# Optimization experiments

Measured on AMD Instinct MI355X. Metric: run time of the kernel, lower is better.

## Reference

```python
import jax, jax.numpy as jnp
import numpy as np

BETA = 0.9
THRESH = 1.0
ALPHA = 2.0  # snntorch ATan surrogate default

@jax.custom_vjp
def atan_spike(x):
    return (x > 0).astype(x.dtype)

def _atan_fwd(x):
    return atan_spike(x), x

def _atan_bwd(x, g):
    # d/dx of snntorch ATan surrogate: (alpha/2) / (1 + (pi/2*alpha*x)^2)
    return (g * (ALPHA / 2) / (1 + (jnp.pi / 2 * ALPHA * x) ** 2),)

atan_spike.defvjp(_atan_fwd, _atan_bwd)

def setup_inputs() -> dict:
    key = jax.random.key(0)
    k1, k2, k3, k4, k5 = jax.random.split(key, 5)
    B, T, F, H, O = 256, 1024, 64, 512, 64
    x = jax.random.normal(k1, (B, T, F), dtype=jnp.float32)
    s_in = 1.0 / np.sqrt(F)
    s_out = 1.0 / np.sqrt(H)
    W_in = jax.random.uniform(k2, (H, F), jnp.float32, -s_in, s_in)
    b_in = jax.random.uniform(k3, (H,), jnp.float32, -s_in, s_in)
    W_out = jax.random.uniform(k4, (O, H), jnp.float32, -s_out, s_out)
    b_out = jax.random.uniform(k5, (O,), jnp.float32, -s_out, s_out)
    return {"x": x, "W_in": W_in, "b_in": b_in, "W_out": W_out, "b_out": b_out}

def reference(x, W_in, b_in, W_out, b_out):
    B, T, F = x.shape
    H = W_in.shape[0]
    O = W_out.shape[0]
    dt = x.dtype
    # precompute input currents for all steps: [T, B, H]
    cur1_all = jnp.einsum('btf,hf->tbh', x, W_in) + b_in

    def step(carry, cur1):
        mem1, mem_out = carry
        # snntorch Leaky(subtract): reset from previous mem (detached),
        # then mem = beta*mem + input - reset*threshold, spike from new mem.
        reset1 = jax.lax.stop_gradient((mem1 > THRESH).astype(dt))
        mem1 = BETA * mem1 + cur1 - reset1 * THRESH
        spk1 = atan_spike(mem1 - THRESH)
        cur_out = spk1 @ W_out.T + b_out
        reset_o = jax.lax.stop_gradient((mem_out > THRESH).astype(dt))
        mem_out = BETA * mem_out + cur_out - reset_o * THRESH
        spk_out = atan_spike(mem_out - THRESH)
        return (mem1, mem_out), (mem_out, spk_out)

    init = (jnp.zeros((B, H), dt), jnp.zeros((B, O), dt))
    _, (mem_rec, spk_rec) = jax.lax.scan(step, init, cur1_all)
    # [T, B, O] -> [B, T, O]
    return mem_rec.transpose(1, 0, 2), spk_rec.transpose(1, 0, 2)
```

## Files before the change

### kernel.cpp

```cpp
#include <hip/hip_runtime.h>


typedef __attribute__((ext_vector_type(16))) float f32x16;

namespace {
constexpr int kB = 256;
constexpr int kT = 1024;
constexpr int kF = 64;
constexpr int kH = 512;
constexpr int kO = 64;
constexpr float kBeta = 0.9f;
constexpr float kThresh = 1.0f;
constexpr int kThreads = 512;
}

#define XV(i) ((i) < 16 ? sx0[(i)] : (i) < 32 ? sx1[(i)-16] \
             : (i) < 48 ? sx2[(i)-32] : sx3[(i)-48])
#define BITF(k) ((((k) < 32 ? (mlo >> (k)) : (mhi >> ((k)-32))) & 1u) \
                 ? 1.0f : 0.0f)

__global__ __launch_bounds__(kThreads, 2)
void snn_fused2(const float* __restrict__ x,
                const float* __restrict__ W_in,
                const float* __restrict__ b_in,
                const float* __restrict__ W_out,
                const float* __restrict__ b_out,
                float* __restrict__ out) {
  const int b = blockIdx.x;
  const int j = threadIdx.x;
  const int o = j & 63;
  const int s = j >> 6;

  __shared__ float red[2][8][64];

  float win[kF];
#pragma unroll
  for (int q = 0; q < 16; ++q) {
    const float4 v = *reinterpret_cast<const float4*>(W_in + j * kF + q * 4);
    win[q * 4 + 0] = v.x; win[q * 4 + 1] = v.y;
    win[q * 4 + 2] = v.z; win[q * 4 + 3] = v.w;
  }
  float wout[64];
#pragma unroll
  for (int q = 0; q < 16; ++q) {
    const float4 v =
        *reinterpret_cast<const float4*>(W_out + o * kH + s * 64 + q * 4);
    wout[q * 4 + 0] = v.x; wout[q * 4 + 1] = v.y;
    wout[q * 4 + 2] = v.z; wout[q * 4 + 3] = v.w;
  }
  const float bin_j = b_in[j];
  const float bout_o = b_out[o];

  float mem1 = 0.0f, rst1 = 0.0f;
  float memo = 0.0f, rsto = 0.0f;
  unsigned long long mask = 0ull;

  const float* xrow = x + (size_t)b * kT * kF;
  float* out_mem = out + (size_t)b * kT * kO + o;
  float* out_spk = out_mem + (size_t)kB * kT * kO;

  f32x16 sx0, sx1, sx2, sx3;

#define ISSUE_X(tt)                                                        \
  do {                                                                     \
    const float* xp = xrow + (size_t)(tt) * kF;                            \
    asm volatile("s_load_dwordx16 %0, %4, 0x0\n\t"                         \
                 "s_load_dwordx16 %1, %4, 0x40\n\t"                        \
                 "s_load_dwordx16 %2, %4, 0x80\n\t"                        \
                 "s_load_dwordx16 %3, %4, 0xc0"                            \
                 : "=&s"(sx0), "=&s"(sx1), "=&s"(sx2), "=&s"(sx3)          \
                 : "s"(xp));                                               \
  } while (0)

#define BARRIER() asm volatile("s_waitcnt lgkmcnt(0)\n\ts_barrier" ::: "memory")

#define PIN_X()                                                            \
  asm volatile("s_waitcnt lgkmcnt(0)"                                      \
               : "+s"(sx0), "+s"(sx1), "+s"(sx2), "+s"(sx3)::"memory")

#define LAYER1()                                                           \
  do {                                                                     \
    float c0 = bin_j, c1 = 0.0f, c2 = 0.0f, c3 = 0.0f;                     \
    _Pragma("unroll") for (int q = 0; q < 16; ++q) {                       \
      c0 = fmaf(XV(4 * q + 0), win[4 * q + 0], c0);                        \
      c1 = fmaf(XV(4 * q + 1), win[4 * q + 1], c1);                        \
      c2 = fmaf(XV(4 * q + 2), win[4 * q + 2], c2);                        \
      c3 = fmaf(XV(4 * q + 3), win[4 * q + 3], c3);                        \
    }                                                                      \
    const float cur1 = (c0 + c1) + (c2 + c3);                              \
    mem1 = kBeta * mem1 + cur1 - rst1;                                     \
    const bool p = mem1 > kThresh;                                         \
    mask = __ballot(p);                                                    \
    rst1 = p ? 1.0f : 0.0f;                                                \
  } while (0)

#define LAYER2(buf)                                                        \
  do {                                                                     \
    const unsigned mlo = (unsigned)mask;                                   \
    const unsigned mhi = (unsigned)(mask >> 32);                           \
    float a0 = 0.0f, a1 = 0.0f, a2 = 0.0f, a3 = 0.0f;                      \
    _Pragma("unroll") for (int q = 0; q < 16; ++q) {                       \
      a0 = fmaf(BITF(4 * q + 0), wout[4 * q + 0], a0);                     \
      a1 = fmaf(BITF(4 * q + 1), wout[4 * q + 1], a1);                     \
      a2 = fmaf(BITF(4 * q + 2), wout[4 * q + 2], a2);                     \
      a3 = fmaf(BITF(4 * q + 3), wout[4 * q + 3], a3);                     \
    }                                                                      \
    red[(buf)][s][o] = (a0 + a1) + (a2 + a3);                              \
  } while (0)

  ISSUE_X(0);
  BARRIER();
  PIN_X();
  LAYER1();

  for (int t = 1; t < kT; ++t) {
    ISSUE_X(t);
    LAYER2((t - 1) & 1);
    BARRIER();
    PIN_X();

    {
      const int buf = (t - 1) & 1;
      float co = bout_o;
#pragma unroll
      for (int s2 = 0; s2 < 8; ++s2) co += red[buf][s2][o];
      memo = kBeta * memo + co - rsto;
      const float so = (memo > kThresh) ? 1.0f : 0.0f;
      rsto = so;
      if (j < kO) {
        out_mem[(t - 1) * kO] = memo;
        out_spk[(t - 1) * kO] = so;
      }
    }

    LAYER1();
  }

  LAYER2((kT - 1) & 1);
  BARRIER();
  {
    const int buf = (kT - 1) & 1;
    float co = bout_o;
#pragma unroll
    for (int s2 = 0; s2 < 8; ++s2) co += red[buf][s2][o];
    memo = kBeta * memo + co - rsto;
    const float so = (memo > kThresh) ? 1.0f : 0.0f;
    if (j < kO) {
      out_mem[(kT - 1) * kO] = memo;
      out_spk[(kT - 1) * kO] = so;
    }
  }

#undef ISSUE_X
#undef BARRIER
#undef PIN_X
#undef LAYER1
#undef LAYER2
}

extern "C" void kernel_launch(void* const* d_in, const int* in_sizes, int n_in,
                              void* d_out, int out_size, void* d_ws,
                              size_t ws_size, hipStream_t stream) {
  const float* x = (const float*)d_in[0];
  const float* W_in = (const float*)d_in[1];
  const float* b_in = (const float*)d_in[2];
  const float* W_out = (const float*)d_in[3];
  const float* b_out = (const float*)d_in[4];
  float* out = (float*)d_out;

  hipLaunchKernelGGL(snn_fused2, dim3(kB), dim3(kThreads), 0, stream,
                     x, W_in, b_in, W_out, b_out, out);
}
```

Baseline: 1.169 ms.

## Prefetch x via vector loads one step ahead and pre-warm cache with a read kernel

Replaces the per-step scalar s_load_dwordx16 fetch of x with 16 float4 vector loads per thread, issued one timestep ahead so the loads overlap the layer-2 work and the barrier. A separate warm-up kernel first streams all of x through the cache so the recurrent kernel's loads hit in L2/MALL. Weights are pinned to registers with empty asm statements, and the output reduction is limited to the first wave instead of being computed by every thread. Every thread now holds 64 extra VGPRs for the x copy, which can raise register pressure, and the warm-up kernel adds a full extra read pass over x.

```diff
diff --git a/kernel.cpp b/kernel.cpp
--- a/kernel.cpp
+++ b/kernel.cpp
@@ -1,7 +1,5 @@
 #include <hip/hip_runtime.h>
 
-
-typedef __attribute__((ext_vector_type(16))) float f32x16;
 
 namespace {
 constexpr int kB = 256;
@@ -14,13 +12,22 @@
 constexpr int kThreads = 512;
 }
 
-#define XV(i) ((i) < 16 ? sx0[(i)] : (i) < 32 ? sx1[(i)-16] \
-             : (i) < 48 ? sx2[(i)-32] : sx3[(i)-48])
+__global__ __launch_bounds__(256)
+void warm_x_kernel(const float4* __restrict__ p, int n4) {
+  float acc = 0.0f;
+  for (int i = blockIdx.x * blockDim.x + threadIdx.x; i < n4;
+       i += gridDim.x * blockDim.x) {
+    const float4 v = p[i];
+    acc += v.x + v.y + v.z + v.w;
+  }
+  asm volatile("" ::"v"(acc));
+}
+
 #define BITF(k) ((((k) < 32 ? (mlo >> (k)) : (mhi >> ((k)-32))) & 1u) \
                  ? 1.0f : 0.0f)
 
 __global__ __launch_bounds__(kThreads, 2)
-void snn_fused2(const float* __restrict__ x,
+void snn_fused4(const float* __restrict__ x,
                 const float* __restrict__ W_in,
                 const float* __restrict__ b_in,
                 const float* __restrict__ W_out,
@@ -34,59 +41,72 @@
   __shared__ float red[2][8][64];
 
   float win[kF];
+  {
+    const float4* wiv = reinterpret_cast<const float4*>(W_in) + j * 16;
 #pragma unroll
-  for (int q = 0; q < 16; ++q) {
-    const float4 v = *reinterpret_cast<const float4*>(W_in + j * kF + q * 4);
-    win[q * 4 + 0] = v.x; win[q * 4 + 1] = v.y;
-    win[q * 4 + 2] = v.z; win[q * 4 + 3] = v.w;
+    for (int q = 0; q < 16; ++q) {
+      const float4 v = wiv[q];
+      win[4 * q + 0] = v.x; win[4 * q + 1] = v.y;
+      win[4 * q + 2] = v.z; win[4 * q + 3] = v.w;
+    }
   }
   float wout[64];
+  {
+    const float4* wov =
+        reinterpret_cast<const float4*>(W_out) + o * 128 + s * 16;
 #pragma unroll
-  for (int q = 0; q < 16; ++q) {
-    const float4 v =
-        *reinterpret_cast<const float4*>(W_out + o * kH + s * 64 + q * 4);
-    wout[q * 4 + 0] = v.x; wout[q * 4 + 1] = v.y;
-    wout[q * 4 + 2] = v.z; wout[q * 4 + 3] = v.w;
+    for (int q = 0; q < 16; ++q) {
+      const float4 v = wov[q];
+      wout[4 * q + 0] = v.x; wout[4 * q + 1] = v.y;
+      wout[4 * q + 2] = v.z; wout[4 * q + 3] = v.w;
+    }
   }
-  const float bin_j = b_in[j];
-  const float bout_o = b_out[o];
+  float bin_j = b_in[j];
+  float bout_o = b_out[o];
+
+#define PIN8(p)                                                            \
+  asm volatile("" : "+v"((p)[0]), "+v"((p)[1]), "+v"((p)[2]),              \
+                    "+v"((p)[3]), "+v"((p)[4]), "+v"((p)[5]),              \
+                    "+v"((p)[6]), "+v"((p)[7]))
+  PIN8(win + 0);  PIN8(win + 8);  PIN8(win + 16); PIN8(win + 24);
+  PIN8(win + 32); PIN8(win + 40); PIN8(win + 48); PIN8(win + 56);
+  PIN8(wout + 0);  PIN8(wout + 8);  PIN8(wout + 16); PIN8(wout + 24);
+  PIN8(wout + 32); PIN8(wout + 40); PIN8(wout + 48); PIN8(wout + 56);
+#undef PIN8
+  asm volatile("" : "+v"(bin_j), "+v"(bout_o));
 
   float mem1 = 0.0f, rst1 = 0.0f;
   float memo = 0.0f, rsto = 0.0f;
   unsigned long long mask = 0ull;
 
-  const float* xrow = x + (size_t)b * kT * kF;
+  const float4* xv = reinterpret_cast<const float4*>(x + (size_t)b * kT * kF);
   float* out_mem = out + (size_t)b * kT * kO + o;
   float* out_spk = out_mem + (size_t)kB * kT * kO;
 
-  f32x16 sx0, sx1, sx2, sx3;
+  float4 x0, x1, x2, x3, x4, x5, x6, x7, x8, x9, x10, x11, x12, x13, x14, x15;
 
-#define ISSUE_X(tt)                                                        \
+#define LOADX(tt)                                                          \
   do {                                                                     \
-    const float* xp = xrow + (size_t)(tt) * kF;                            \
-    asm volatile("s_load_dwordx16 %0, %4, 0x0\n\t"                         \
-                 "s_load_dwordx16 %1, %4, 0x40\n\t"                        \
-                 "s_load_dwordx16 %2, %4, 0x80\n\t"                        \
-                 "s_load_dwordx16 %3, %4, 0xc0"                            \
-                 : "=&s"(sx0), "=&s"(sx1), "=&s"(sx2), "=&s"(sx3)          \
-                 : "s"(xp));                                               \
+    const float4* xp = xv + (size_t)(tt) * 16;                             \
+    x0 = xp[0]; x1 = xp[1]; x2 = xp[2]; x3 = xp[3];                        \
+    x4 = xp[4]; x5 = xp[5]; x6 = xp[6]; x7 = xp[7];                        \
+    x8 = xp[8]; x9 = xp[9]; x10 = xp[10]; x11 = xp[11];                    \
+    x12 = xp[12]; x13 = xp[13]; x14 = xp[14]; x15 = xp[15];                \
   } while (0)
 
 #define BARRIER() asm volatile("s_waitcnt lgkmcnt(0)\n\ts_barrier" ::: "memory")
 
-#define PIN_X()                                                            \
-  asm volatile("s_waitcnt lgkmcnt(0)"                                      \
-               : "+s"(sx0), "+s"(sx1), "+s"(sx2), "+s"(sx3)::"memory")
+#define L1Q(q)                                                             \
+  c0 = fmaf(x##q.x, win[4 * q + 0], c0);                                   \
+  c1 = fmaf(x##q.y, win[4 * q + 1], c1);                                   \
+  c2 = fmaf(x##q.z, win[4 * q + 2], c2);                                   \
+  c3 = fmaf(x##q.w, win[4 * q + 3], c3);
 
 #define LAYER1()                                                           \
   do {                                                                     \
     float c0 = bin_j, c1 = 0.0f, c2 = 0.0f, c3 = 0.0f;                     \
-    _Pragma("unroll") for (int q = 0; q < 16; ++q) {                       \
-      c0 = fmaf(XV(4 * q + 0), win[4 * q + 0], c0);                        \
-      c1 = fmaf(XV(4 * q + 1), win[4 * q + 1], c1);                        \
-      c2 = fmaf(XV(4 * q + 2), win[4 * q + 2], c2);                        \
-      c3 = fmaf(XV(4 * q + 3), win[4 * q + 3], c3);                        \
-    }                                                                      \
+    L1Q(0) L1Q(1) L1Q(2) L1Q(3) L1Q(4) L1Q(5) L1Q(6) L1Q(7)                \
+    L1Q(8) L1Q(9) L1Q(10) L1Q(11) L1Q(12) L1Q(13) L1Q(14) L1Q(15)          \
     const float cur1 = (c0 + c1) + (c2 + c3);                              \
     mem1 = kBeta * mem1 + cur1 - rst1;                                     \
     const bool p = mem1 > kThresh;                                         \
@@ -94,68 +114,63 @@
     rst1 = p ? 1.0f : 0.0f;                                                \
   } while (0)
 
+#define L2Q(q)                                                             \
+  a0 = fmaf(BITF(4 * q + 0), wout[4 * q + 0], a0);                         \
+  a1 = fmaf(BITF(4 * q + 1), wout[4 * q + 1], a1);                         \
+  a2 = fmaf(BITF(4 * q + 2), wout[4 * q + 2], a2);                         \
+  a3 = fmaf(BITF(4 * q + 3), wout[4 * q + 3], a3);
+
 #define LAYER2(buf)                                                        \
   do {                                                                     \
     const unsigned mlo = (unsigned)mask;                                   \
     const unsigned mhi = (unsigned)(mask >> 32);                           \
     float a0 = 0.0f, a1 = 0.0f, a2 = 0.0f, a3 = 0.0f;                      \
-    _Pragma("unroll") for (int q = 0; q < 16; ++q) {                       \
-      a0 = fmaf(BITF(4 * q + 0), wout[4 * q + 0], a0);                     \
-      a1 = fmaf(BITF(4 * q + 1), wout[4 * q + 1], a1);                     \
-      a2 = fmaf(BITF(4 * q + 2), wout[4 * q + 2], a2);                     \
-      a3 = fmaf(BITF(4 * q + 3), wout[4 * q + 3], a3);                     \
-    }                                                                      \
+    L2Q(0) L2Q(1) L2Q(2) L2Q(3) L2Q(4) L2Q(5) L2Q(6) L2Q(7)                \
+    L2Q(8) L2Q(9) L2Q(10) L2Q(11) L2Q(12) L2Q(13) L2Q(14) L2Q(15)         \
     red[(buf)][s][o] = (a0 + a1) + (a2 + a3);                              \
   } while (0)
 
-  ISSUE_X(0);
-  BARRIER();
-  PIN_X();
+#define REDUCE_STORE(tt)                                                   \
+  do {                                                                     \
+    if (s == 0) {                                                          \
+      const int buf = (tt) & 1;                                            \
+      float co = bout_o;                                                   \
+      co += red[buf][0][o]; co += red[buf][1][o];                          \
+      co += red[buf][2][o]; co += red[buf][3][o];                          \
+      co += red[buf][4][o]; co += red[buf][5][o];                          \
+      co += red[buf][6][o]; co += red[buf][7][o];                          \
+      memo = kBeta * memo + co - rsto;                                     \
+      const float so = (memo > kThresh) ? 1.0f : 0.0f;                     \
+      rsto = so;                                                           \
+      out_mem[(tt) * kO] = memo;                                           \
+      out_spk[(tt) * kO] = so;                                             \
+    }                                                                      \
+  } while (0)
+
+  LOADX(0);
   LAYER1();
+  LOADX(1);
 
   for (int t = 1; t < kT; ++t) {
-    ISSUE_X(t);
     LAYER2((t - 1) & 1);
     BARRIER();
-    PIN_X();
-
-    {
-      const int buf = (t - 1) & 1;
-      float co = bout_o;
-#pragma unroll
-      for (int s2 = 0; s2 < 8; ++s2) co += red[buf][s2][o];
-      memo = kBeta * memo + co - rsto;
-      const float so = (memo > kThresh) ? 1.0f : 0.0f;
-      rsto = so;
-      if (j < kO) {
-        out_mem[(t - 1) * kO] = memo;
-        out_spk[(t - 1) * kO] = so;
-      }
-    }
-
+    REDUCE_STORE(t - 1);
     LAYER1();
+    const int tn = (t + 1 < kT) ? (t + 1) : (kT - 1);
+    LOADX(tn);
   }
 
   LAYER2((kT - 1) & 1);
   BARRIER();
-  {
-    const int buf = (kT - 1) & 1;
-    float co = bout_o;
-#pragma unroll
-    for (int s2 = 0; s2 < 8; ++s2) co += red[buf][s2][o];
-    memo = kBeta * memo + co - rsto;
-    const float so = (memo > kThresh) ? 1.0f : 0.0f;
-    if (j < kO) {
-      out_mem[(kT - 1) * kO] = memo;
-      out_spk[(kT - 1) * kO] = so;
-    }
-  }
+  REDUCE_STORE(kT - 1);
 
-#undef ISSUE_X
+#undef LOADX
 #undef BARRIER
-#undef PIN_X
+#undef L1Q
 #undef LAYER1
+#undef L2Q
 #undef LAYER2
+#undef REDUCE_STORE
 }
 
 extern "C" void kernel_launch(void* const* d_in, const int* in_sizes, int n_in,
@@ -168,6 +183,9 @@
   const float* b_out = (const float*)d_in[4];
   float* out = (float*)d_out;
 
-  hipLaunchKernelGGL(snn_fused2, dim3(kB), dim3(kThreads), 0, stream,
+  const int n4 = kB * kT * kF / 4;
+  hipLaunchKernelGGL(warm_x_kernel, dim3(1024), dim3(256), 0, stream,
+                     (const float4*)x, n4);
+  hipLaunchKernelGGL(snn_fused4, dim3(kB), dim3(kThreads), 0, stream,
                      x, W_in, b_in, W_out, b_out, out);
 }
```

Measured after the change: 2.624 ms. 2.25x slower.
